# Kernel tuning notes

Measured on AMD Instinct MI355X. Metric: run time of the kernel, lower is better.

Reference implementation:

```python
import jax, jax.numpy as jnp
import numpy as np

LENGTHS = [1024, 768, 896, 512, 1024, 640, 1024, 768, 512, 896, 1024, 704]  # sum = 9792
EMBED, HEADS = 1024, 16
HDIM = EMBED // HEADS  # 64
ROPE_BASE = 10000.0


def _rotate_half(x):
    half = x.shape[-1] // 2
    return jnp.concatenate([-x[..., half:], x[..., :half]], axis=-1)


def setup_inputs() -> dict:
    key = jax.random.key(0)
    ks = jax.random.split(key, 8)
    T = sum(LENGTHS)
    hidden = jax.random.normal(ks[0], (T, EMBED), jnp.float32)
    # RoPE cos/sin: positions restart at 0 within each packed segment
    pos = np.concatenate([np.arange(l) for l in LENGTHS]).astype(np.float32)  # [T]
    inv_freq = 1.0 / (ROPE_BASE ** (np.arange(0, HDIM, 2, dtype=np.float32) / HDIM))
    freqs = np.outer(pos, inv_freq)                       # [T, HDIM//2]
    emb = np.concatenate([freqs, freqs], axis=-1)         # [T, HDIM]
    cos = jnp.asarray(np.cos(emb), jnp.float32)
    sin = jnp.asarray(np.sin(emb), jnp.float32)
    s = 0.02
    q_w = jax.random.normal(ks[1], (EMBED, EMBED), jnp.float32) * s
    k_w = jax.random.normal(ks[2], (EMBED, EMBED), jnp.float32) * s
    v_w = jax.random.normal(ks[3], (EMBED, EMBED), jnp.float32) * s
    out_w = jax.random.normal(ks[4], (EMBED, EMBED), jnp.float32) * s
    q_b = jax.random.normal(ks[5], (EMBED,), jnp.float32) * s
    v_b = jax.random.normal(ks[6], (EMBED,), jnp.float32) * s
    out_b = jax.random.normal(ks[7], (EMBED,), jnp.float32) * s
    return {
        "hidden_states": hidden, "cos": cos, "sin": sin,
        "q_w": q_w, "q_b": q_b, "k_w": k_w, "v_w": v_w, "v_b": v_b,
        "out_w": out_w, "out_b": out_b,
        "seq_len": jnp.array(LENGTHS, jnp.int32),
        "max_seqlen": 1024,
    }


def reference(hidden_states, cos, sin, q_w, q_b, k_w, v_w, v_b, out_w, out_b,
              seq_len, max_seqlen):
    T, D = hidden_states.shape
    H, Dh = HEADS, D // HEADS
    B = seq_len.shape[0]
    L = max_seqlen  # static python int

    # Projections (torch Linear: y = x @ W.T + b; k_proj has no bias)
    q = (hidden_states @ q_w.T + q_b).reshape(T, H, Dh)
    k = (hidden_states @ k_w.T).reshape(T, H, Dh)
    v = (hidden_states @ v_w.T + v_b).reshape(T, H, Dh)

    # Inline RoPE (cos/sin broadcast over heads)
    c = cos[:, None, :]
    s = sin[:, None, :]
    q = q * c + _rotate_half(q) * s
    k = k * c + _rotate_half(k) * s

    # Gather packed tokens into padded [B, L, H, Dh] (honors ragged structure:
    # no [T, T] dense score matrix, only per-segment [L, L] blocks)
    cu = jnp.concatenate([jnp.zeros((1,), seq_len.dtype), jnp.cumsum(seq_len)])[:-1]  # [B] starts
    ar = jnp.arange(L)
    idx = cu[:, None] + ar[None, :]                 # [B, L] token ids
    valid = ar[None, :] < seq_len[:, None]          # [B, L]
    idxc = jnp.minimum(idx, T - 1)
    qp = q[idxc]                                    # [B, L, H, Dh]
    kp = k[idxc]
    vp = v[idxc]

    scale = 1.0 / jnp.sqrt(jnp.float32(Dh))
    scores = jnp.einsum('blhd,bmhd->bhlm', qp, kp) * scale  # [B, H, L, L]
    causal = ar[:, None] >= ar[None, :]             # [L, L]
    mask = valid[:, None, None, :] & causal[None, None, :, :]
    scores = jnp.where(mask, scores, jnp.float32(-1e30))
    probs = jax.nn.softmax(scores, axis=-1)
    attn = jnp.einsum('bhlm,bmhd->blhd', probs, vp).reshape(B, L, D)

    # Scatter valid tokens back to packed layout [T, D]
    attn = attn * valid[..., None].astype(attn.dtype)
    flat = jnp.zeros((T, D), attn.dtype).at[idxc.reshape(-1)].add(attn.reshape(-1, D))
    return flat @ out_w.T + out_b
```

## Files before the change

### kernel.cpp

```cpp
#include <hip/hip_runtime.h>

typedef __bf16 bf16;
typedef __bf16 bf16x8 __attribute__((ext_vector_type(8)));
typedef __bf16 bf16x4 __attribute__((ext_vector_type(4)));
typedef float  f32x4  __attribute__((ext_vector_type(4)));

#define T_TOTAL 9792
#define EMBED   1024
#define NHEAD   16
#define HDIM    64

__constant__ int c_seq_start13[13] = {0,1024,1792,2688,3200,4224,4864,5888,6656,7168,8064,9088,9792};
__constant__ int c_qtiles_cum[13] = {0,8,14,21,25,33,38,46,52,56,63,71,77};

typedef __attribute__((address_space(1))) unsigned int gu32;
typedef __attribute__((address_space(3))) unsigned int lu32;

__device__ __forceinline__ void load_lds16(const void* g, void* l) {
    __builtin_amdgcn_global_load_lds((gu32*)g, (lu32*)l, 16, 0, 0);
}

__device__ __forceinline__ f32x4 mfma16(bf16x8 a, bf16x8 b, f32x4 c) {
    return __builtin_amdgcn_mfma_f32_16x16x32_bf16(a, b, c, 0, 0, 0);
}

__device__ __forceinline__ int xcd_chunk(int bid, int chunk) {
    return (bid & 7) * chunk + (bid >> 3);
}

struct CvtArgs {
    const void* src[10];
    bf16*       dst[10];
    int         n[10];
    int         cum[10];
};

__global__ void to_bf16_fused(CvtArgs a, const unsigned short* __restrict__ disc)
{
    const bool f32 = (disc[0] == 0);
    const int blk = blockIdx.x;
    int seg = 0;
    #pragma unroll
    for (int i = 1; i < 10; ++i) if (blk >= a.cum[i]) seg = i;
    int i0 = (blk - a.cum[seg]) * 2048 + threadIdx.x * 8;
    if (i0 >= a.n[seg]) return;
    bf16x8 o;
    if (f32) {
        const float4* s = (const float4*)((const float*)a.src[seg] + i0);
        float4 x = s[0], y = s[1];
        o[0]=(bf16)x.x; o[1]=(bf16)x.y; o[2]=(bf16)x.z; o[3]=(bf16)x.w;
        o[4]=(bf16)y.x; o[5]=(bf16)y.y; o[6]=(bf16)y.z; o[7]=(bf16)y.w;
    } else {
        o = *(const bf16x8*)((const bf16*)a.src[seg] + i0);
    }
    *(bf16x8*)(a.dst[seg] + i0) = o;
}

__device__ __forceinline__
void gemm_core(const bf16* __restrict__ A, const bf16* __restrict__ W,
               int M, int m0, int n0, f32x4 (&acc)[4][4],
               bf16* lA, bf16* lB)
{
    const int tid  = threadIdx.x;
    const int wave = tid >> 6, lane = tid & 63;
    const int lrow = lane >> 3;
    const int gsw  = (lane & 7) ^ lrow;
    const int ln   = lane & 15, lq = lane >> 4;
    const int e7   = ln & 7;
    const int wm = (wave & 1) * 64,  wn = (wave >> 1) * 64;

    for (int k0 = 0; k0 < 1024; k0 += 64) {
        __syncthreads();
        for (int j = 0; j < 4; ++j) {
            int r = j * 32 + wave * 8;
            int gr = m0 + r + lrow; if (gr > M - 1) gr = M - 1;
            load_lds16(A + (size_t)gr * EMBED + k0 + gsw * 8, &lA[r * 64]);
            load_lds16(W + (size_t)(n0 + r + lrow) * EMBED + k0 + gsw * 8, &lB[r * 64]);
        }
        __syncthreads();
        #pragma unroll
        for (int kb = 0; kb < 2; ++kb) {
            bf16x8 af[4], bfr[4];
            #pragma unroll
            for (int i = 0; i < 4; ++i)
                af[i]  = *(const bf16x8*)&lA[(wm + i * 16 + ln) * 64 + (((kb * 4 + lq) ^ e7) * 8)];
            #pragma unroll
            for (int i = 0; i < 4; ++i)
                bfr[i] = *(const bf16x8*)&lB[(wn + i * 16 + ln) * 64 + (((kb * 4 + lq) ^ e7) * 8)];
            #pragma unroll
            for (int mi = 0; mi < 4; ++mi)
                #pragma unroll
                for (int ni = 0; ni < 4; ++ni)
                    acc[mi][ni] = mfma16(af[mi], bfr[ni], acc[mi][ni]);
        }
    }
}

__device__ __forceinline__ void map_block(int L, int NY, int& x, int& y)
{
    const int per = 8 * NY;
    const int full = 9 * per;
    if (L < full) { int sc = L / per, rem = L % per; x = sc * 8 + (rem & 7); y = rem >> 3; }
    else          { int rem = L - full; x = 72 + rem % 5; y = rem / 5; }
}

__global__ __launch_bounds__(256, 2)
void gemm_qkv(const bf16* __restrict__ A,
              const bf16* __restrict__ Wq, const bf16* __restrict__ Wk,
              const bf16* __restrict__ Wv, const bf16* __restrict__ qb,
              const bf16* __restrict__ vb,
              const bf16* __restrict__ cosb, const bf16* __restrict__ sinb,
              bf16* __restrict__ Cq, bf16* __restrict__ Ck,
              bf16* __restrict__ Vt, int M)
{
    __shared__ __align__(16) bf16 lA[128 * 64];
    __shared__ __align__(16) bf16 lB[128 * 64];

    int x, yy;
    map_block(xcd_chunk(blockIdx.x, 231), 24, x, yy);
    const int which = yy >> 3;
    const int m0 = x * 128, n0 = (yy & 7) * 128;

    const bf16* W = (which == 0) ? Wq : (which == 1) ? Wk : Wv;
    f32x4 acc[4][4] = {};
    gemm_core(A, W, M, m0, n0, acc, lA, lB);

    const int tid  = threadIdx.x;
    const int wave = tid >> 6, lane = tid & 63;
    const int ln   = lane & 15, lq = lane >> 4;
    const int wm = (wave & 1) * 64,  wn = (wave >> 1) * 64;

    if (which < 2) {
        bf16* C = (which == 0) ? Cq : Ck;
        const bf16* bias = (which == 0) ? qb : nullptr;
        #pragma unroll
        for (int mi = 0; mi < 4; ++mi) {
            int trow = m0 + wm + mi * 16 + lq * 4;
            if (trow >= M) continue;
            #pragma unroll
            for (int ni = 0; ni < 2; ++ni) {
                int d    = ni * 16 + ln;
                int col0 = n0 + wn + d;
                int col1 = col0 + 32;
                float b0 = bias ? (float)bias[col0] : 0.0f;
                float b1 = bias ? (float)bias[col1] : 0.0f;
                #pragma unroll
                for (int r = 0; r < 4; ++r) {
                    int t = trow + r;
                    float c = (float)cosb[t * HDIM + d];
                    float s = (float)sinb[t * HDIM + d];
                    float x0 = acc[mi][ni][r] + b0;
                    float x1 = acc[mi][ni + 2][r] + b1;
                    C[(size_t)t * EMBED + col0] = (bf16)(x0 * c - x1 * s);
                    C[(size_t)t * EMBED + col1] = (bf16)(x1 * c + x0 * s);
                }
            }
        }
    } else {
        const int hd0 = n0 + wn;
        #pragma unroll
        for (int mi = 0; mi < 4; ++mi) {
            int trow = m0 + wm + mi * 16 + lq * 4;
            if (trow >= M) continue;
            #pragma unroll
            for (int ni = 0; ni < 4; ++ni) {
                int d = ni * 16 + ln;
                float bv = (float)vb[hd0 + d];
                bf16x4 o;
                #pragma unroll
                for (int r = 0; r < 4; ++r) o[r] = (bf16)(acc[mi][ni][r] + bv);
                *(bf16x4*)&Vt[(size_t)(hd0 + d) * T_TOTAL + trow] = o;
            }
        }
    }
}

__global__ __launch_bounds__(256, 2)
void gemm_out(const bf16* __restrict__ A, const bf16* __restrict__ W,
              const bf16* __restrict__ bias, void* __restrict__ out, int M,
              const unsigned short* __restrict__ disc)
{
    __shared__ __align__(16) bf16 lA[128 * 64];
    __shared__ __align__(16) bf16 lB[128 * 64];

    int x, yy;
    map_block(xcd_chunk(blockIdx.x, 77), 8, x, yy);
    const int m0 = x * 128, n0 = yy * 128;

    f32x4 acc[4][4] = {};
    gemm_core(A, W, M, m0, n0, acc, lA, lB);

    const bool f32 = (disc[0] == 0);
    const int tid  = threadIdx.x;
    const int wave = tid >> 6, lane = tid & 63;
    const int ln   = lane & 15, lq = lane >> 4;
    const int wm = (wave & 1) * 64,  wn = (wave >> 1) * 64;

    #pragma unroll
    for (int mi = 0; mi < 4; ++mi) {
        int trow = m0 + wm + mi * 16 + lq * 4;
        if (trow >= M) continue;
        #pragma unroll
        for (int ni = 0; ni < 4; ++ni) {
            int col = n0 + wn + ni * 16 + ln;
            float bv = (float)bias[col];
            #pragma unroll
            for (int r = 0; r < 4; ++r) {
                float v = acc[mi][ni][r] + bv;
                size_t idx = (size_t)(trow + r) * EMBED + col;
                if (f32) ((float*)out)[idx] = v;
                else     ((bf16*)out)[idx]  = (bf16)v;
            }
        }
    }
}

__global__ __launch_bounds__(512, 6)
void attn_kernel(const bf16* __restrict__ Q, const bf16* __restrict__ K,
                 const bf16* __restrict__ Vt, bf16* __restrict__ O)
{
    __shared__ __align__(16) bf16 sK[2][64 * 64];
    __shared__ __align__(16) bf16 sV[2][64 * 64];
    __shared__ __align__(16) bf16 sQP[8 * 16 * 72];

    const int tid  = threadIdx.x;
    const int wave = tid >> 6, lane = tid & 63;
    const int lrow = lane >> 3;
    const int gsw  = (lane & 7) ^ lrow;
    const int ln   = lane & 15, lq = lane >> 4;
    const int e7   = ln & 7;

    const int swz = xcd_chunk(blockIdx.x, 154);
    const int h  = swz / 77;
    const int qx = swz - h * 77;

    int b = 0;
    #pragma unroll
    for (int i = 1; i < 13; ++i) if (qx >= c_qtiles_cum[i]) b = i;
    const int qt   = qx - c_qtiles_cum[b];
    const int s0   = c_seq_start13[b];
    const int len  = c_seq_start13[b + 1] - s0;
    const int t0   = s0 + qt * 128;
    const int vrows = len - qt * 128;
    const int lastrow = (vrows < 128 ? vrows : 128) - 1;
    const int jmax = (qt * 128 + lastrow) >> 6;

    for (int p = 0; p < 2; ++p) {
        int r = p * 64 + wave * 8 + lrow;
        int qr = t0 + r; if (qr > T_TOTAL - 1) qr = T_TOTAL - 1;
        load_lds16(Q + (size_t)qr * EMBED + h * HDIM + gsw * 8, &sQP[r * 64]);
    }
    {
        int r = wave * 8 + lrow;
        load_lds16(K  + (size_t)(s0 + r) * EMBED + h * HDIM + gsw * 8, &sK[0][r * 64]);
        load_lds16(Vt + (size_t)(h * HDIM + r) * T_TOTAL + s0 + gsw * 8, &sV[0][r * 64]);
    }

    bf16x8 qf[2];
    f32x4 oacc[4] = {};
    float m_i = -1e30f, l_i = 0.0f;
    const float sc = 0.125f * 1.44269504088896f;
    const int q_loc = wave * 16 + ln;
    bf16* sP = &sQP[wave * 16 * 72];

    for (int j = 0; j <= jmax; ++j) {
        __syncthreads();
        const int cur = j & 1;
        if (j == 0) {
            qf[0] = *(const bf16x8*)&sQP[q_loc * 64 + ((0 + lq) ^ e7) * 8];
            qf[1] = *(const bf16x8*)&sQP[q_loc * 64 + ((4 + lq) ^ e7) * 8];
            __syncthreads();
        }
        if (j < jmax) {
            const int kvb = s0 + (j + 1) * 64;
            const int nxt = cur ^ 1;
            int r = wave * 8 + lrow;
            load_lds16(K  + (size_t)(kvb + r) * EMBED + h * HDIM + gsw * 8, &sK[nxt][r * 64]);
            load_lds16(Vt + (size_t)(h * HDIM + r) * T_TOTAL + kvb + gsw * 8, &sV[nxt][r * 64]);
        }

        f32x4 s[4] = {};
        #pragma unroll
        for (int kk = 0; kk < 2; ++kk)
            #pragma unroll
            for (int ni = 0; ni < 4; ++ni) {
                bf16x8 kf = *(const bf16x8*)&sK[cur][(ni * 16 + ln) * 64 + (((kk * 4 + lq) ^ e7) * 8)];
                s[ni] = mfma16(kf, qf[kk], s[ni]);
            }

        float pb[4][4];
        if (j >= 2 * qt) {
            const int off = (j - 2 * qt) * 64;
            #pragma unroll
            for (int ni = 0; ni < 4; ++ni)
                #pragma unroll
                for (int r = 0; r < 4; ++r) {
                    int kv = off + ni * 16 + lq * 4 + r;
                    pb[ni][r] = (kv <= q_loc) ? s[ni][r] * sc : -1e30f;
                }
        } else {
            #pragma unroll
            for (int ni = 0; ni < 4; ++ni)
                #pragma unroll
                for (int r = 0; r < 4; ++r)
                    pb[ni][r] = s[ni][r] * sc;
        }

        float mx = pb[0][0];
        #pragma unroll
        for (int ni = 0; ni < 4; ++ni)
            #pragma unroll
            for (int r = 0; r < 4; ++r) mx = fmaxf(mx, pb[ni][r]);
        mx = fmaxf(mx, __shfl_xor(mx, 16));
        mx = fmaxf(mx, __shfl_xor(mx, 32));

        if (!__all(mx <= m_i + 8.0f)) {
            float mnew  = fmaxf(m_i, mx);
            float alpha = exp2f(m_i - mnew);
            l_i *= alpha;
            #pragma unroll
            for (int d = 0; d < 4; ++d)
                #pragma unroll
                for (int r = 0; r < 4; ++r) oacc[d][r] *= alpha;
            m_i = mnew;
        }

        float rs = 0.0f;
        #pragma unroll
        for (int ni = 0; ni < 4; ++ni)
            #pragma unroll
            for (int r = 0; r < 4; ++r) {
                float pe = exp2f(pb[ni][r] - m_i);
                pb[ni][r] = pe;
                rs += pe;
            }
        rs += __shfl_xor(rs, 16);
        rs += __shfl_xor(rs, 32);
        l_i += rs;

        #pragma unroll
        for (int ni = 0; ni < 4; ++ni) {
            bf16x4 w4;
            #pragma unroll
            for (int r = 0; r < 4; ++r) w4[r] = (bf16)pb[ni][r];
            *(bf16x4*)&sP[ln * 72 + ni * 16 + lq * 4] = w4;
        }
        asm volatile("s_waitcnt lgkmcnt(0)" ::: "memory");

        #pragma unroll
        for (int kk = 0; kk < 2; ++kk) {
            bf16x8 pf = *(const bf16x8*)&sP[ln * 72 + kk * 32 + lq * 8];
            #pragma unroll
            for (int d = 0; d < 4; ++d) {
                bf16x8 vf = *(const bf16x8*)&sV[cur][(d * 16 + ln) * 64 + (((kk * 4 + lq) ^ e7) * 8)];
                oacc[d] = mfma16(vf, pf, oacc[d]);
            }
        }
    }

    if (q_loc < vrows) {
        const float inv = 1.0f / l_i;
        const size_t row = (size_t)(t0 + q_loc) * EMBED + h * HDIM;
        #pragma unroll
        for (int d = 0; d < 4; ++d) {
            bf16x4 o4;
            #pragma unroll
            for (int r = 0; r < 4; ++r) o4[r] = (bf16)(oacc[d][r] * inv);
            *(bf16x4*)&O[row + d * 16 + lq * 4] = o4;
        }
    }
}

extern "C" void kernel_launch(void* const* d_in, const int* in_sizes, int n_in,
                              void* d_out, int out_size, void* d_ws, size_t ws_size,
                              hipStream_t stream)
{
    const unsigned short* disc = (const unsigned short*)d_in[1];

    const size_t SZ  = (size_t)T_TOTAL * EMBED;
    const size_t CS  = (size_t)T_TOTAL * HDIM;
    const size_t WSZ = (size_t)EMBED * EMBED;

    bf16* p = (bf16*)d_ws;
    bf16* ch   = p; p += SZ;
    bf16* ccos = p; p += CS;
    bf16* csin = p; p += CS;
    bf16* cqw  = p; p += WSZ;
    bf16* ckw  = p; p += WSZ;
    bf16* cvw  = p; p += WSZ;
    bf16* cow  = p; p += WSZ;
    bf16* cqb  = p; p += EMBED;
    bf16* cvb  = p; p += EMBED;
    bf16* cob  = p; p += EMBED;
    bf16* wq   = p; p += SZ;
    bf16* wk   = p; p += SZ;
    bf16* wvt  = p; p += SZ;

    CvtArgs ca;
    const void* srcs[10] = {d_in[0], d_in[1], d_in[2], d_in[3], d_in[5],
                            d_in[6], d_in[8], d_in[4], d_in[7], d_in[9]};
    bf16* dsts[10] = {ch, ccos, csin, cqw, ckw, cvw, cow, cqb, cvb, cob};
    int   ns[10]   = {(int)SZ, (int)CS, (int)CS, (int)WSZ, (int)WSZ,
                      (int)WSZ, (int)WSZ, EMBED, EMBED, EMBED};
    int cum = 0;
    for (int i = 0; i < 10; ++i) {
        ca.src[i] = srcs[i]; ca.dst[i] = dsts[i]; ca.n[i] = ns[i];
        ca.cum[i] = cum;
        cum += (ns[i] + 2047) / 2048;
    }
    to_bf16_fused<<<cum, 256, 0, stream>>>(ca, disc);

    gemm_qkv<<<77 * 24, 256, 0, stream>>>(ch, cqw, ckw, cvw, cqb, cvb,
                                          ccos, csin, wq, wk, wvt, T_TOTAL);
    attn_kernel<<<1232, 512, 0, stream>>>(wq, wk, wvt, wq);
    gemm_out<<<77 * 8, 256, 0, stream>>>(wq, cow, cob, d_out, T_TOTAL, disc);
}
```

Baseline: 287.8 us.

## Skip bf16 conversion when inputs are bf16, split QKV GEMM, reverse attention tile order

Adds a host check on input byte sizes. When every input is already bf16, the conversion kernel is skipped and the input buffers are used directly. The fused QKV GEMM is split into a Q/K kernel with RoPE and a separate V kernel that writes the transposed layout, which removes the three-way branch inside the epilogue. Attention blocks now take query tiles in reverse order so the heavier tiles late in each segment start first, at the cost of one extra kernel launch.

```diff
diff --git a/kernel.cpp b/kernel.cpp
--- a/kernel.cpp
+++ b/kernel.cpp
@@ -105,23 +105,21 @@
 }
 
 __global__ __launch_bounds__(256, 2)
-void gemm_qkv(const bf16* __restrict__ A,
-              const bf16* __restrict__ Wq, const bf16* __restrict__ Wk,
-              const bf16* __restrict__ Wv, const bf16* __restrict__ qb,
-              const bf16* __restrict__ vb,
-              const bf16* __restrict__ cosb, const bf16* __restrict__ sinb,
-              bf16* __restrict__ Cq, bf16* __restrict__ Ck,
-              bf16* __restrict__ Vt, int M)
+void gemm_qk(const bf16* __restrict__ A,
+             const bf16* __restrict__ Wq, const bf16* __restrict__ Wk,
+             const bf16* __restrict__ qb,
+             const bf16* __restrict__ cosb, const bf16* __restrict__ sinb,
+             bf16* __restrict__ Cq, bf16* __restrict__ Ck, int M)
 {
     __shared__ __align__(16) bf16 lA[128 * 64];
     __shared__ __align__(16) bf16 lB[128 * 64];
 
     int x, yy;
-    map_block(xcd_chunk(blockIdx.x, 231), 24, x, yy);
+    map_block(xcd_chunk(blockIdx.x, 154), 16, x, yy);
     const int which = yy >> 3;
     const int m0 = x * 128, n0 = (yy & 7) * 128;
 
-    const bf16* W = (which == 0) ? Wq : (which == 1) ? Wk : Wv;
+    const bf16* W = which ? Wk : Wq;
     f32x4 acc[4][4] = {};
     gemm_core(A, W, M, m0, n0, acc, lA, lB);
 
@@ -130,47 +128,65 @@
     const int ln   = lane & 15, lq = lane >> 4;
     const int wm = (wave & 1) * 64,  wn = (wave >> 1) * 64;
 
-    if (which < 2) {
-        bf16* C = (which == 0) ? Cq : Ck;
-        const bf16* bias = (which == 0) ? qb : nullptr;
-        #pragma unroll
-        for (int mi = 0; mi < 4; ++mi) {
-            int trow = m0 + wm + mi * 16 + lq * 4;
-            if (trow >= M) continue;
-            #pragma unroll
-            for (int ni = 0; ni < 2; ++ni) {
-                int d    = ni * 16 + ln;
-                int col0 = n0 + wn + d;
-                int col1 = col0 + 32;
-                float b0 = bias ? (float)bias[col0] : 0.0f;
-                float b1 = bias ? (float)bias[col1] : 0.0f;
-                #pragma unroll
-                for (int r = 0; r < 4; ++r) {
-                    int t = trow + r;
-                    float c = (float)cosb[t * HDIM + d];
-                    float s = (float)sinb[t * HDIM + d];
-                    float x0 = acc[mi][ni][r] + b0;
-                    float x1 = acc[mi][ni + 2][r] + b1;
-                    C[(size_t)t * EMBED + col0] = (bf16)(x0 * c - x1 * s);
-                    C[(size_t)t * EMBED + col1] = (bf16)(x1 * c + x0 * s);
-                }
+    bf16* C = which ? Ck : Cq;
+    const bf16* bias = which ? nullptr : qb;
+    #pragma unroll
+    for (int mi = 0; mi < 4; ++mi) {
+        int trow = m0 + wm + mi * 16 + lq * 4;
+        if (trow >= M) continue;
+        #pragma unroll
+        for (int ni = 0; ni < 2; ++ni) {
+            int d    = ni * 16 + ln;
+            int col0 = n0 + wn + d;
+            int col1 = col0 + 32;
+            float b0 = bias ? (float)bias[col0] : 0.0f;
+            float b1 = bias ? (float)bias[col1] : 0.0f;
+            #pragma unroll
+            for (int r = 0; r < 4; ++r) {
+                int t = trow + r;
+                float c = (float)cosb[t * HDIM + d];
+                float s = (float)sinb[t * HDIM + d];
+                float x0 = acc[mi][ni][r] + b0;
+                float x1 = acc[mi][ni + 2][r] + b1;
+                C[(size_t)t * EMBED + col0] = (bf16)(x0 * c - x1 * s);
+                C[(size_t)t * EMBED + col1] = (bf16)(x1 * c + x0 * s);
             }
         }
-    } else {
-        const int hd0 = n0 + wn;
-        #pragma unroll
-        for (int mi = 0; mi < 4; ++mi) {
-            int trow = m0 + wm + mi * 16 + lq * 4;
-            if (trow >= M) continue;
-            #pragma unroll
-            for (int ni = 0; ni < 4; ++ni) {
-                int d = ni * 16 + ln;
-                float bv = (float)vb[hd0 + d];
-                bf16x4 o;
-                #pragma unroll
-                for (int r = 0; r < 4; ++r) o[r] = (bf16)(acc[mi][ni][r] + bv);
-                *(bf16x4*)&Vt[(size_t)(hd0 + d) * T_TOTAL + trow] = o;
-            }
+    }
+}
+
+__global__ __launch_bounds__(256, 2)
+void gemm_v(const bf16* __restrict__ A, const bf16* __restrict__ Wv,
+            const bf16* __restrict__ vb, bf16* __restrict__ Vt, int M)
+{
+    __shared__ __align__(16) bf16 lA[128 * 64];
+    __shared__ __align__(16) bf16 lB[128 * 64];
+
+    int x, yy;
+    map_block(xcd_chunk(blockIdx.x, 77), 8, x, yy);
+    const int m0 = x * 128, n0 = yy * 128;
+
+    f32x4 acc[4][4] = {};
+    gemm_core(A, Wv, M, m0, n0, acc, lA, lB);
+
+    const int tid  = threadIdx.x;
+    const int wave = tid >> 6, lane = tid & 63;
+    const int ln   = lane & 15, lq = lane >> 4;
+    const int wm = (wave & 1) * 64,  wn = (wave >> 1) * 64;
+
+    const int hd0 = n0 + wn;
+    #pragma unroll
+    for (int mi = 0; mi < 4; ++mi) {
+        int trow = m0 + wm + mi * 16 + lq * 4;
+        if (trow >= M) continue;
+        #pragma unroll
+        for (int ni = 0; ni < 4; ++ni) {
+            int d = ni * 16 + ln;
+            float bv = (float)vb[hd0 + d];
+            bf16x4 o;
+            #pragma unroll
+            for (int r = 0; r < 4; ++r) o[r] = (bf16)(acc[mi][ni][r] + bv);
+            *(bf16x4*)&Vt[(size_t)(hd0 + d) * T_TOTAL + trow] = o;
         }
     }
 }
@@ -232,7 +248,7 @@
 
     const int swz = xcd_chunk(blockIdx.x, 154);
     const int h  = swz / 77;
-    const int qx = swz - h * 77;
+    const int qx = 76 - (swz - h * 77);
 
     int b = 0;
     #pragma unroll
@@ -396,22 +412,37 @@
     bf16* wk   = p; p += SZ;
     bf16* wvt  = p; p += SZ;
 
-    CvtArgs ca;
-    const void* srcs[10] = {d_in[0], d_in[1], d_in[2], d_in[3], d_in[5],
-                            d_in[6], d_in[8], d_in[4], d_in[7], d_in[9]};
-    bf16* dsts[10] = {ch, ccos, csin, cqw, ckw, cvw, cow, cqb, cvb, cob};
-    int   ns[10]   = {(int)SZ, (int)CS, (int)CS, (int)WSZ, (int)WSZ,
-                      (int)WSZ, (int)WSZ, EMBED, EMBED, EMBED};
-    int cum = 0;
-    for (int i = 0; i < 10; ++i) {
-        ca.src[i] = srcs[i]; ca.dst[i] = dsts[i]; ca.n[i] = ns[i];
-        ca.cum[i] = cum;
-        cum += (ns[i] + 2047) / 2048;
-    }
-    to_bf16_fused<<<cum, 256, 0, stream>>>(ca, disc);
-
-    gemm_qkv<<<77 * 24, 256, 0, stream>>>(ch, cqw, ckw, cvw, cqb, cvb,
-                                          ccos, csin, wq, wk, wvt, T_TOTAL);
+    const bool all_bf16 =
+        in_sizes[0] == (int)(SZ * 2)  && in_sizes[1] == (int)(CS * 2) &&
+        in_sizes[2] == (int)(CS * 2)  && in_sizes[3] == (int)(WSZ * 2) &&
+        in_sizes[5] == (int)(WSZ * 2) && in_sizes[6] == (int)(WSZ * 2) &&
+        in_sizes[8] == (int)(WSZ * 2) && in_sizes[4] == (int)(EMBED * 2) &&
+        in_sizes[7] == (int)(EMBED * 2) && in_sizes[9] == (int)(EMBED * 2);
+
+    if (all_bf16) {
+        ch   = (bf16*)d_in[0]; ccos = (bf16*)d_in[1]; csin = (bf16*)d_in[2];
+        cqw  = (bf16*)d_in[3]; ckw  = (bf16*)d_in[5]; cvw  = (bf16*)d_in[6];
+        cow  = (bf16*)d_in[8]; cqb  = (bf16*)d_in[4]; cvb  = (bf16*)d_in[7];
+        cob  = (bf16*)d_in[9];
+    } else {
+        CvtArgs ca;
+        const void* srcs[10] = {d_in[0], d_in[1], d_in[2], d_in[3], d_in[5],
+                                d_in[6], d_in[8], d_in[4], d_in[7], d_in[9]};
+        bf16* dsts[10] = {ch, ccos, csin, cqw, ckw, cvw, cow, cqb, cvb, cob};
+        int   ns[10]   = {(int)SZ, (int)CS, (int)CS, (int)WSZ, (int)WSZ,
+                          (int)WSZ, (int)WSZ, EMBED, EMBED, EMBED};
+        int cum = 0;
+        for (int i = 0; i < 10; ++i) {
+            ca.src[i] = srcs[i]; ca.dst[i] = dsts[i]; ca.n[i] = ns[i];
+            ca.cum[i] = cum;
+            cum += (ns[i] + 2047) / 2048;
+        }
+        to_bf16_fused<<<cum, 256, 0, stream>>>(ca, disc);
+    }
+
+    gemm_qk<<<77 * 16, 256, 0, stream>>>(ch, cqw, ckw, cqb, ccos, csin,
+                                         wq, wk, T_TOTAL);
+    gemm_v<<<77 * 8, 256, 0, stream>>>(ch, cvw, cvb, wvt, T_TOTAL);
     attn_kernel<<<1232, 512, 0, stream>>>(wq, wk, wvt, wq);
     gemm_out<<<77 * 8, 256, 0, stream>>>(wq, cow, cob, d_out, T_TOTAL, disc);
 }
```

Result: slower. 303.8 us (+5.6%).
